# Kernel tuning notes

Hardware: AMD Instinct MI355X
Metric: run time of the kernel (lower is better)

## Reference

```python
import jax, jax.numpy as jnp
import numpy as np

N_FEATS = 9       # OGB atom feature columns
VOCAB = 119       # per-feature embedding vocab (max OGB atom vocab)
HIDDEN = 128
NUM_HEADS = 8
HEAD_DIM = HIDDEN // NUM_HEADS


def setup_inputs() -> dict:
    key = jax.random.key(0)
    ks = jax.random.split(key, 12)
    N, K = 50000, 16
    X = jax.random.randint(ks[0], (N, N_FEATS), 0, VOCAB)
    nbr_idx = jax.random.randint(ks[1], (N, K), 0, N)
    nbr_mask = jax.random.randint(ks[2], (N, K), 0, 2).astype(bool)
    atom_emb = jax.random.normal(ks[3], (N_FEATS, VOCAB, HIDDEN), jnp.float32) * 0.02
    s = 1.0 / np.sqrt(HIDDEN)
    Wq = jax.random.normal(ks[4], (HIDDEN, HIDDEN), jnp.float32) * s
    bq = jnp.zeros((HIDDEN,), jnp.float32)
    Wk = jax.random.normal(ks[5], (HIDDEN, HIDDEN), jnp.float32) * s
    bk = jnp.zeros((HIDDEN,), jnp.float32)
    Wv = jax.random.normal(ks[6], (HIDDEN, HIDDEN), jnp.float32) * s
    bv = jnp.zeros((HIDDEN,), jnp.float32)
    return {"X": X, "nbr_idx": nbr_idx, "nbr_mask": nbr_mask,
            "atom_emb": atom_emb, "Wq": Wq, "bq": bq,
            "Wk": Wk, "bk": bk, "Wv": Wv, "bv": bv}


def reference(X, nbr_idx, nbr_mask, atom_emb, Wq, bq, Wk, bk, Wv, bv):
    N = X.shape[0]
    # AtomEncoder: sum per-feature embedding lookups -> [N, HIDDEN]
    h = jnp.sum(atom_emb[jnp.arange(N_FEATS)[None, :], X], axis=1)
    scaling = HEAD_DIM ** -0.5
    q = (h @ Wq + bq).reshape(N, NUM_HEADS, HEAD_DIM) * scaling
    k = (h @ Wk + bk).reshape(N, NUM_HEADS, HEAD_DIM)
    v = (h @ Wv + bv).reshape(N, NUM_HEADS, HEAD_DIM)
    # ELL-format sparse attention: gather padded neighbor k/v -> [N, K, H, D]
    k_n = k[nbr_idx]
    v_n = v[nbr_idx]
    scores = jnp.einsum('nhd,nkhd->nkh', q, k_n)          # [N, K, H]
    scores = jnp.where(nbr_mask[..., None], scores, -1e9)
    attn = jax.nn.softmax(scores, axis=1)                 # softmax over neighbors
    out = jnp.einsum('nkh,nkhd->nhd', attn, v_n)          # [N, H, D]
    return out.reshape(N, HIDDEN)
```

## Files before the change

### kernel.cpp

```cpp
#include <hip/hip_runtime.h>
#include <hip/hip_bf16.h>

#define NFEAT 9
#define VOCAB 119
#define HIDDEN 128
#define NHEAD 8
#define HDIM 16
#define KNBR 16

typedef __attribute__((ext_vector_type(8))) short short8;
typedef __attribute__((ext_vector_type(4))) float f32x4;

__global__ void fill_kernel(float* out, int n, float val) {
    int i = blockIdx.x * blockDim.x + threadIdx.x;
    if (i < n) out[i] = val;
}

__global__ __launch_bounds__(256) void wt_kernel(
    const float* __restrict__ Wq, const float* __restrict__ Wk,
    const float* __restrict__ Wv, short* __restrict__ Wt)
{
    int mat = blockIdx.x >> 2, tile = blockIdx.x & 3;
    const float* W = (mat == 0) ? Wq : (mat == 1) ? Wk : Wv;
    __shared__ float ls[32 * HIDDEN];
    int tid = threadIdx.x;
    int cc0 = tile * 32;
    #pragma unroll
    for (int j = 0; j < 16; ++j) {
        int idx = j * 256 + tid;
        ls[idx] = W[(size_t)cc0 * HIDDEN + idx];
    }
    __syncthreads();
    int c = tid & 127, hf = tid >> 7;
    unsigned int ob[8];
    #pragma unroll
    for (int j = 0; j < 8; ++j) {
        int ccl = hf * 16 + 2 * j;
        __hip_bfloat16 b0 = __float2bfloat16(ls[ccl * HIDDEN + c]);
        __hip_bfloat16 b1 = __float2bfloat16(ls[(ccl + 1) * HIDDEN + c]);
        ob[j] = (unsigned int)*reinterpret_cast<unsigned short*>(&b0)
              | ((unsigned int)*reinterpret_cast<unsigned short*>(&b1) << 16);
    }
    unsigned int* dst = reinterpret_cast<unsigned int*>(
        Wt + (size_t)mat * HIDDEN * HIDDEN + (size_t)c * HIDDEN + cc0 + hf * 16);
    #pragma unroll
    for (int j = 0; j < 8; ++j) dst[j] = ob[j];
}

#define MT 64
#define HBS 136

__global__ __launch_bounds__(256) void qkv_kernel(
    const int* __restrict__ X, const float* __restrict__ emb,
    const short* __restrict__ Wt,
    const float* __restrict__ bq, const float* __restrict__ bk,
    const float* __restrict__ bv,
    float* __restrict__ qf, __hip_bfloat16* __restrict__ kv, int N)
{
    __shared__ __align__(16) short hb[MT * HBS];
    __shared__ __align__(16) short Wb[HIDDEN * HBS];
    __shared__ int xs[MT * NFEAT];

    const int tid = threadIdx.x;
    const int n0 = blockIdx.x * MT;

    for (int i = tid; i < MT * NFEAT; i += 256) {
        int n = n0 + i / NFEAT;
        int v = (n < N) ? X[(size_t)n * NFEAT + (i % NFEAT)] : 0;
        xs[i] = min(max(v, 0), VOCAB - 1);
    }
    __syncthreads();

    const int c = tid & 127, half = tid >> 7;
    for (int i = 0; i < MT / 2; ++i) {
        int nl = half * (MT / 2) + i;
        float acc = 0.f;
        #pragma unroll
        for (int f = 0; f < NFEAT; ++f)
            acc += emb[((size_t)f * VOCAB + xs[nl * NFEAT + f]) * HIDDEN + c];
        reinterpret_cast<__hip_bfloat16*>(hb)[nl * HBS + c] = __float2bfloat16(acc);
    }

    const int wave = tid >> 6, lane = tid & 63;
    const int l15 = lane & 15, quad = lane >> 4;
    const int mloc = wave * 16 + l15;

    for (int mat = 0; mat < 3; ++mat) {
        __syncthreads();
        const uint4* src = reinterpret_cast<const uint4*>(Wt + (size_t)mat * HIDDEN * HIDDEN);
        #pragma unroll
        for (int j = 0; j < 8; ++j) {
            int idx = j * 256 + tid;
            int r = idx >> 4, o = idx & 15;
            *reinterpret_cast<uint4*>(&Wb[r * HBS + o * 8]) = src[idx];
        }
        __syncthreads();

        short8 a[4];
        #pragma unroll
        for (int k0 = 0; k0 < 4; ++k0)
            a[k0] = *reinterpret_cast<const short8*>(&hb[mloc * HBS + k0 * 32 + quad * 8]);

        const float* bias = (mat == 0) ? bq : (mat == 1) ? bk : bv;
        #pragma unroll
        for (int nt = 0; nt < 8; ++nt) {
            f32x4 acc = {0.f, 0.f, 0.f, 0.f};
            int n = nt * 16 + l15;
            #pragma unroll
            for (int k0 = 0; k0 < 4; ++k0) {
                short8 b = *reinterpret_cast<const short8*>(&Wb[n * HBS + k0 * 32 + quad * 8]);
                acc = __builtin_amdgcn_mfma_f32_16x16x32_bf16(a[k0], b, acc, 0, 0, 0);
            }
            float bb = bias[n];
            #pragma unroll
            for (int r = 0; r < 4; ++r) {
                int node = n0 + wave * 16 + quad * 4 + r;
                if (node < N) {
                    float val = acc[r] + bb;
                    if (mat == 0)      qf[(size_t)node * HIDDEN + n] = val * 0.25f;
                    else if (mat == 1) kv[(size_t)node * 256 + n] = __float2bfloat16(val);
                    else               kv[(size_t)node * 256 + 128 + n] = __float2bfloat16(val);
                }
            }
        }
    }
}

#define NPB2 2
#define KV_LDS_STRIDE 264

__global__ __launch_bounds__(256) void attn_kernel(
    const int* __restrict__ nbr_idx, const int* __restrict__ nbr_mask,
    const float* __restrict__ qf, const __hip_bfloat16* __restrict__ kv,
    float* __restrict__ out, int N)
{
    __shared__ __hip_bfloat16 kvl[NPB2][KNBR][KV_LDS_STRIDE];
    __shared__ float ql[NPB2][HIDDEN];
    __shared__ float sl[NPB2][KNBR][NHEAD + 1];
    __shared__ float el[NPB2][KNBR][NHEAD + 1];
    __shared__ int idxl[NPB2][KNBR];
    __shared__ int mskl[NPB2][KNBR];

    const int tid = threadIdx.x;
    const int local = tid >> 7;
    const int t = tid & 127;
    int n = blockIdx.x * NPB2 + local;
    if (n >= N) n = N - 1;

    ql[local][t] = qf[(size_t)n * HIDDEN + t];
    if (t < KNBR) {
        int iv = nbr_idx[(size_t)n * KNBR + t];
        idxl[local][t] = min(max(iv, 0), N - 1);
        mskl[local][t] = nbr_mask[(size_t)n * KNBR + t];
    }
    __syncthreads();

    #pragma unroll
    for (int kk = 0; kk < KNBR; ++kk) {
        size_t row = (size_t)idxl[local][kk] * 256;
        reinterpret_cast<unsigned int*>(&kvl[local][kk][0])[t] =
            reinterpret_cast<const unsigned int*>(kv + row)[t];
    }
    __syncthreads();

    const int kk = t >> 3, hh = t & 7;
    float s = 0.f;
    {
        const __hip_bfloat162* kp =
            reinterpret_cast<const __hip_bfloat162*>(&kvl[local][kk][hh * HDIM]);
        const float* qp = &ql[local][hh * HDIM];
        #pragma unroll
        for (int d2 = 0; d2 < HDIM / 2; ++d2) {
            float2 kf = __bfloat1622float2(kp[d2]);
            s += qp[2 * d2] * kf.x + qp[2 * d2 + 1] * kf.y;
        }
    }
    if (!mskl[local][kk]) s = -1e9f;
    sl[local][kk][hh] = s;
    __syncthreads();

    float mx = -3.0e38f;
    #pragma unroll
    for (int j = 0; j < KNBR; ++j) mx = fmaxf(mx, sl[local][j][hh]);
    float e = __expf(s - mx);
    el[local][kk][hh] = e;
    __syncthreads();
    float denom = 0.f;
    #pragma unroll
    for (int j = 0; j < KNBR; ++j) denom += el[local][j][hh];
    sl[local][kk][hh] = e / denom;
    __syncthreads();

    const int h2 = t >> 4, dd = t & 15;
    float o = 0.f;
    #pragma unroll
    for (int j = 0; j < KNBR; ++j) {
        float a = sl[local][j][h2];
        float vv = __bfloat162float(kvl[local][j][HIDDEN + h2 * HDIM + dd]);
        o += a * vv;
    }
    out[(size_t)n * HIDDEN + t] = o;
}

extern "C" void kernel_launch(void* const* d_in, const int* in_sizes, int n_in,
                              void* d_out, int out_size, void* d_ws, size_t ws_size,
                              hipStream_t stream)
{
    float* out = (float*)d_out;

    bool ok = (n_in == 10);
    int N = ok ? in_sizes[0] / NFEAT : 0;
    ok = ok && N > 0 && in_sizes[0] == N * NFEAT
            && in_sizes[1] == N * KNBR
            && in_sizes[2] == N * KNBR
            && in_sizes[3] == NFEAT * VOCAB * HIDDEN
            && in_sizes[4] == HIDDEN * HIDDEN && in_sizes[5] == HIDDEN
            && in_sizes[6] == HIDDEN * HIDDEN && in_sizes[7] == HIDDEN
            && in_sizes[8] == HIDDEN * HIDDEN && in_sizes[9] == HIDDEN
            && out_size == N * HIDDEN;
    if (!ok) {
        fill_kernel<<<(out_size + 255) / 256, 256, 0, stream>>>(out, out_size, 0.0f);
        return;
    }
    size_t need = (size_t)N * 1024 + 3 * HIDDEN * HIDDEN * sizeof(short);
    if (ws_size < need) {
        fill_kernel<<<(out_size + 255) / 256, 256, 0, stream>>>(out, out_size, 1.0f);
        return;
    }

    const int* X        = (const int*)d_in[0];
    const int* nbr_idx  = (const int*)d_in[1];
    const int* nbr_mask = (const int*)d_in[2];
    const float* emb = (const float*)d_in[3];
    const float* Wq  = (const float*)d_in[4];
    const float* bq  = (const float*)d_in[5];
    const float* Wk  = (const float*)d_in[6];
    const float* bk  = (const float*)d_in[7];
    const float* Wv  = (const float*)d_in[8];
    const float* bv  = (const float*)d_in[9];

    float* qf = (float*)d_ws;
    __hip_bfloat16* kv =
        (__hip_bfloat16*)((char*)d_ws + (size_t)N * HIDDEN * sizeof(float));
    short* Wt = (short*)((char*)d_ws + (size_t)N * 1024);

    wt_kernel<<<12, 256, 0, stream>>>(Wq, Wk, Wv, Wt);
    qkv_kernel<<<(N + MT - 1) / MT, 256, 0, stream>>>(
        X, emb, Wt, bq, bk, bv, qf, kv, N);
    attn_kernel<<<(N + NPB2 - 1) / NPB2, 256, 0, stream>>>(
        nbr_idx, nbr_mask, qf, kv, out, N);
}
```

Measured before the change: 197.5 us.

## Vectorize embedding gather and use direct global-to-LDS loads for neighbor KV

The atom-embedding sum in the QKV kernel now has each thread gather float4 chunks instead of single floats, and writes packed bf16 pairs to shared memory. This cuts the number of load instructions for the embedding lookup. In the attention kernel, neighbor K/V rows are copied straight into shared memory with 16-byte global_load_lds operations, bypassing registers. The padded LDS row stride is dropped to fit that instruction's contiguous per-wave layout, which may add bank conflicts on later shared-memory reads.

After: 187.4 us. 5.1% less time.

```diff
diff --git a/kernel.cpp b/kernel.cpp
--- a/kernel.cpp
+++ b/kernel.cpp
@@ -11,6 +11,11 @@
 typedef __attribute__((ext_vector_type(8))) short short8;
 typedef __attribute__((ext_vector_type(4))) float f32x4;
 
+__device__ __forceinline__ void load_lds16(const void* g, void* l) {
+    __builtin_amdgcn_global_load_lds((const __attribute__((address_space(1))) void*)g,
+                                     (__attribute__((address_space(3))) void*)l, 16, 0, 0);
+}
+
 __global__ void fill_kernel(float* out, int n, float val) {
     int i = blockIdx.x * blockDim.x + threadIdx.x;
     if (i < n) out[i] = val;
@@ -71,14 +76,26 @@
     }
     __syncthreads();
 
-    const int c = tid & 127, half = tid >> 7;
-    for (int i = 0; i < MT / 2; ++i) {
-        int nl = half * (MT / 2) + i;
-        float acc = 0.f;
-        #pragma unroll
-        for (int f = 0; f < NFEAT; ++f)
-            acc += emb[((size_t)f * VOCAB + xs[nl * NFEAT + f]) * HIDDEN + c];
-        reinterpret_cast<__hip_bfloat16*>(hb)[nl * HBS + c] = __float2bfloat16(acc);
+    {
+        const int cg = tid & 31;
+        const int slot = tid >> 5;
+        #pragma unroll
+        for (int i = 0; i < 8; ++i) {
+            int nl = slot * 8 + i;
+            float4 acc = {0.f, 0.f, 0.f, 0.f};
+            #pragma unroll
+            for (int f = 0; f < NFEAT; ++f) {
+                const float4 e = *reinterpret_cast<const float4*>(
+                    &emb[((size_t)f * VOCAB + xs[nl * NFEAT + f]) * HIDDEN + cg * 4]);
+                acc.x += e.x; acc.y += e.y; acc.z += e.z; acc.w += e.w;
+            }
+            __hip_bfloat162 p0 = __float22bfloat162_rn(make_float2(acc.x, acc.y));
+            __hip_bfloat162 p1 = __float22bfloat162_rn(make_float2(acc.z, acc.w));
+            uint2 u;
+            u.x = *reinterpret_cast<unsigned int*>(&p0);
+            u.y = *reinterpret_cast<unsigned int*>(&p1);
+            *reinterpret_cast<uint2*>(&hb[nl * HBS + cg * 4]) = u;
+        }
     }
 
     const int wave = tid >> 6, lane = tid & 63;
@@ -127,14 +144,13 @@
 }
 
 #define NPB2 2
-#define KV_LDS_STRIDE 264
 
 __global__ __launch_bounds__(256) void attn_kernel(
     const int* __restrict__ nbr_idx, const int* __restrict__ nbr_mask,
     const float* __restrict__ qf, const __hip_bfloat16* __restrict__ kv,
     float* __restrict__ out, int N)
 {
-    __shared__ __hip_bfloat16 kvl[NPB2][KNBR][KV_LDS_STRIDE];
+    __shared__ __align__(16) __hip_bfloat16 kvl[NPB2][KNBR][256];
     __shared__ float ql[NPB2][HIDDEN];
     __shared__ float sl[NPB2][KNBR][NHEAD + 1];
     __shared__ float el[NPB2][KNBR][NHEAD + 1];
@@ -155,11 +171,16 @@
     }
     __syncthreads();
 
-    #pragma unroll
-    for (int kk = 0; kk < KNBR; ++kk) {
-        size_t row = (size_t)idxl[local][kk] * 256;
-        reinterpret_cast<unsigned int*>(&kvl[local][kk][0])[t] =
-            reinterpret_cast<const unsigned int*>(kv + row)[t];
+    {
+        const int w2 = t >> 6;
+        const int l = t & 63;
+        #pragma unroll
+        for (int j = 0; j < 4; ++j) {
+            int r = 4 * j + 2 * w2 + (l >> 5);
+            const short* src = (const short*)kv
+                + (size_t)idxl[local][r] * 256 + (size_t)(l & 31) * 8;
+            load_lds16(src, &kvl[local][4 * j + 2 * w2][0]);
+        }
     }
     __syncthreads();
 
```
